# Performance work log

Hardware: AMD Instinct MI355X
Metric: run time of the kernel (lower is better)

## Reference

```python
import jax, jax.numpy as jnp
import numpy as np

B, T, D = 2, 128, 1024
H, R, Dk, Dv = 8, 8, 64, 64


def setup_inputs() -> dict:
    key = jax.random.key(0)
    ks = jax.random.split(key, 11)
    w = lambda k, shp: jax.random.normal(k, shp, dtype=jnp.float32) * 0.02
    return {
        "hidden_states": jax.random.normal(ks[0], (B, T, D), dtype=jnp.float32),
        "Wq": w(ks[1], (D, H * Dk)),
        "Wk": w(ks[2], (D, H * Dk)),
        "Wv": w(ks[3], (D, H * Dv)),
        "Wb": w(ks[4], (D, H * R)),
        "Wtg": w(ks[5], (D, H * R)),
        "mode_logits": jax.random.normal(ks[6], (H, R), dtype=jnp.float32) * 0.1,
        "log_decay": jax.random.normal(ks[7], (H, R), dtype=jnp.float32) * 0.1,
        "omega_log_scale": jax.random.normal(ks[8], (H, R), dtype=jnp.float32) * 0.1,
        "Wg": w(ks[9], (D, H * Dv)),
        "Wo": w(ks[10], (H * Dv, D)),
    }


def _forward(x, Wq, Wk, Wv, Wb, Wtg, mode_logits, log_decay, omega_log_scale, Wg, Wo):
    b, t, _ = x.shape
    # projections
    q = (x @ Wq).reshape(b, t, H, Dk)
    k = (x @ Wk).reshape(b, t, H, Dk)
    v = (x @ Wv).reshape(b, t, H, Dv)
    beta = jax.nn.sigmoid((x @ Wb).reshape(b, t, H, R))
    tg = jax.nn.sigmoid((x @ Wtg).reshape(b, t, H, R))
    # spectral mode parameters
    pair_idx = jnp.arange(0, Dk, 2, dtype=jnp.float32)
    inv_freq = 1.0 / (10000.0 ** (pair_idx / Dk))            # [Dk/2]
    omega = jnp.exp(omega_log_scale)[..., None] * inv_freq    # [H,R,Dk/2]
    omega_full = jnp.repeat(omega, 2, axis=-1)                # [H,R,Dk] (repeat_interleave)
    cos_w = jnp.cos(omega_full)[None, :, :, None, :]          # [1,H,R,1,Dk]
    sin_w = jnp.sin(omega_full)[None, :, :, None, :]
    rho = jnp.exp(-jax.nn.softplus(log_decay))                # [H,R]
    mode_w = jax.nn.softmax(mode_logits, axis=-1)             # [H,R]

    # time-major for scan
    qT = jnp.moveaxis(q, 1, 0)
    kT = jnp.moveaxis(k, 1, 0)
    vT = jnp.moveaxis(v, 1, 0)
    betaT = jnp.moveaxis(beta, 1, 0)
    tgT = jnp.moveaxis(tg, 1, 0)

    def step(carry, xs):
        sr, si = carry                      # [B,H,R,Dv,Dk] each
        q_t, k_t, v_t, b_t, g_t = xs
        decay = (g_t * rho)[..., None, None]            # [B,H,R,1,1]
        rot_r = decay * (cos_w * sr - sin_w * si)
        rot_i = decay * (sin_w * sr + cos_w * si)
        pred = jnp.einsum('bhrvk,bhk->bhrv', rot_r, k_t)
        err = v_t[:, :, None, :] - pred                  # [B,H,R,Dv]
        write = err[..., None] * k_t[:, :, None, None, :]
        sr_new = rot_r + b_t[..., None, None] * write
        read = jnp.einsum('bhrvk,bhk->bhrv', sr_new, q_t)
        y = jnp.einsum('bhrv,hr->bhv', read, mode_w)     # [B,H,Dv]
        return (sr_new, rot_i), y

    s0 = jnp.zeros((b, H, R, Dv, Dk), dtype=x.dtype)
    _, ys = jax.lax.scan(step, (s0, s0), (qT, kT, vT, betaT, tgT))
    o = jnp.moveaxis(ys, 0, 1)                           # [B,T,H,Dv]
    gate = jax.nn.sigmoid((x @ Wg).reshape(b, t, H, Dv))
    o = (o * gate).reshape(b, t, H * Dv)
    return o @ Wo


def reference(hidden_states, Wq, Wk, Wv, Wb, Wtg, mode_logits, log_decay,
              omega_log_scale, Wg, Wo):
    return _forward(hidden_states, Wq, Wk, Wv, Wb, Wtg, mode_logits,
                    log_decay, omega_log_scale, Wg, Wo)
```

## Files before the change

kernel.cpp:

```cpp
#include <hip/hip_runtime.h>
#include <math.h>

#define T_ 128
#define NPROJ 2176
#define CH 32

typedef __attribute__((ext_vector_type(8))) short short8;
typedef __attribute__((ext_vector_type(4))) float float4v;
typedef __attribute__((ext_vector_type(2))) float float2v;

__device__ __forceinline__ ushort f2bf(float x) {
    unsigned u = __float_as_uint(x);
    u += 0x7FFF + ((u >> 16) & 1);
    return (ushort)(u >> 16);
}

template<int CTRL>
__device__ __forceinline__ float dpp_add(float x) {
    int xi = __float_as_int(x);
    int yi = __builtin_amdgcn_update_dpp(xi, xi, CTRL, 0xF, 0xF, false);
    return x + __int_as_float(yi);
}

__global__ __launch_bounds__(256) void prep_kernel(
    const float* __restrict__ x,
    const float* __restrict__ Wq, const float* __restrict__ Wk,
    const float* __restrict__ Wv, const float* __restrict__ Wb,
    const float* __restrict__ Wtg, const float* __restrict__ Wg,
    const float* __restrict__ Wo,
    const float* __restrict__ mode_logits, const float* __restrict__ log_decay,
    const float* __restrict__ ols,
    float* __restrict__ cosw, float* __restrict__ sinw,
    float* __restrict__ rho, float* __restrict__ modew,
    ushort* __restrict__ xb, ushort* __restrict__ wtb, ushort* __restrict__ wotb,
    float* __restrict__ Acomb)
{
    __shared__ ushort tile[64][68];
    const int blk = blockIdx.x, tid = threadIdx.x;
    if (blk < 16) {
        int idx = blk * 256 + tid;
        if (idx >= 64 * 64) return;
        int t = idx >> 6;
        int k = idx & 63;
        int h = t >> 3;
        if (k == 0) {
            float ld = log_decay[t];
            rho[t] = 1.0f / (1.0f + expf(ld));
            float m = -1e30f;
            for (int i = 0; i < 8; i++) m = fmaxf(m, mode_logits[h * 8 + i]);
            float sum = 0.0f;
            for (int i = 0; i < 8; i++) sum += expf(mode_logits[h * 8 + i] - m);
            modew[t] = expf(mode_logits[t] - m) / sum;
        }
        float osc = expf(ols[t]);
        int p = k >> 1;
        float invf = expf(-((float)(2 * p) / 64.0f) * logf(10000.0f));
        float w = osc * invf;
        cosw[idx] = cosf(w);
        sinw[idx] = sinf(w);
        return;
    }
    if (blk < 80) {
        int base = (blk - 16) * 4096 + tid * 16;
        float4 f0 = *(const float4*)&x[base];
        float4 f1 = *(const float4*)&x[base + 4];
        float4 f2 = *(const float4*)&x[base + 8];
        float4 f3 = *(const float4*)&x[base + 12];
        short8 o0, o1;
        o0[0]=f2bf(f0.x); o0[1]=f2bf(f0.y); o0[2]=f2bf(f0.z); o0[3]=f2bf(f0.w);
        o0[4]=f2bf(f1.x); o0[5]=f2bf(f1.y); o0[6]=f2bf(f1.z); o0[7]=f2bf(f1.w);
        o1[0]=f2bf(f2.x); o1[1]=f2bf(f2.y); o1[2]=f2bf(f2.z); o1[3]=f2bf(f2.w);
        o1[4]=f2bf(f3.x); o1[5]=f2bf(f3.y); o1[6]=f2bf(f3.z); o1[7]=f2bf(f3.w);
        *(short8*)&xb[base] = o0;
        *(short8*)&xb[base + 8] = o1;
        return;
    }
    if (blk >= 752) {
        int base = (blk - 752) * 4096 + tid * 16;
        float4 z = make_float4(0.f, 0.f, 0.f, 0.f);
        *(float4*)&Acomb[base] = z;
        *(float4*)&Acomb[base + 4] = z;
        *(float4*)&Acomb[base + 8] = z;
        *(float4*)&Acomb[base + 12] = z;
        return;
    }
    const float* src; int ld, c0, n0, k0, ldd; ushort* dst;
    if (blk < 624) {
        int b3 = blk - 80; int nt = b3 >> 4, kt = b3 & 15;
        n0 = nt * 64; k0 = kt * 64;
        if (n0 < 512)       { src = Wq;  c0 = n0;        ld = 512; }
        else if (n0 < 1024) { src = Wk;  c0 = n0 - 512;  ld = 512; }
        else if (n0 < 1536) { src = Wv;  c0 = n0 - 1024; ld = 512; }
        else if (n0 < 1600) { src = Wb;  c0 = n0 - 1536; ld = 64;  }
        else if (n0 < 1664) { src = Wtg; c0 = n0 - 1600; ld = 64;  }
        else                { src = Wg;  c0 = n0 - 1664; ld = 512; }
        dst = wtb; ldd = 1024;
    } else {
        int b4 = blk - 624; int nt = b4 >> 3, kt = b4 & 7;
        n0 = nt * 64; k0 = kt * 64;
        src = Wo; c0 = n0; ld = 1024; dst = wotb; ldd = 512;
    }
    #pragma unroll
    for (int rep = 0; rep < 4; rep++) {
        int k = rep * 16 + (tid >> 4);
        int nc = (tid & 15) * 4;
        float4 f = *(const float4*)&src[(size_t)(k0 + k) * ld + c0 + nc];
        tile[nc + 0][k] = f2bf(f.x);
        tile[nc + 1][k] = f2bf(f.y);
        tile[nc + 2][k] = f2bf(f.z);
        tile[nc + 3][k] = f2bf(f.w);
    }
    __syncthreads();
    #pragma unroll
    for (int rep = 0; rep < 4; rep++) {
        int n = rep * 16 + (tid >> 4);
        int kc = (tid & 15) * 4;
        uint2 uu = *(const uint2*)&tile[n][kc];
        *(uint2*)&dst[(size_t)(n0 + n) * ldd + k0 + kc] = uu;
    }
}

__global__ __launch_bounds__(256, 2) void proj_mfma(const ushort* __restrict__ Ab,
        const ushort* __restrict__ BTb, const float* __restrict__ rho,
        float* __restrict__ proj)
{
    __shared__ ushort sA[2][64][40];
    __shared__ ushort sB[2][64][40];
    const int n0 = blockIdx.x * 64, m0 = blockIdx.y * 64;
    const int tid = threadIdx.x;
    const int lane = tid & 63, w = tid >> 6;
    const int wm = w & 1, wn = w >> 1;
    const int l16 = lane & 15, quad = lane >> 4;
    const int srow = tid >> 2, skq = (tid & 3) * 8;
    const ushort* Ag = Ab + (size_t)(m0 + srow) * 1024 + skq;
    const ushort* Bg = BTb + (size_t)(n0 + srow) * 1024 + skq;
    short8 raA = *(const short8*)Ag;
    short8 rbA = *(const short8*)Bg;
    short8 raB = *(const short8*)(Ag + 32);
    short8 rbB = *(const short8*)(Bg + 32);
    float4v acc00 = {0,0,0,0}, acc01 = {0,0,0,0}, acc10 = {0,0,0,0}, acc11 = {0,0,0,0};
    for (int kt = 0; kt < 32; kt += 2) {
        *(short8*)&sA[0][srow][skq] = raA;
        *(short8*)&sB[0][srow][skq] = rbA;
        __syncthreads();
        if (kt + 2 < 32) {
            raA = *(const short8*)(Ag + (kt + 2) * 32);
            rbA = *(const short8*)(Bg + (kt + 2) * 32);
        }
        {
            short8 a0 = *(const short8*)&sA[0][wm * 32 + l16][quad * 8];
            short8 a1 = *(const short8*)&sA[0][wm * 32 + 16 + l16][quad * 8];
            short8 b0 = *(const short8*)&sB[0][wn * 32 + l16][quad * 8];
            short8 b1 = *(const short8*)&sB[0][wn * 32 + 16 + l16][quad * 8];
            acc00 = __builtin_amdgcn_mfma_f32_16x16x32_bf16(a0, b0, acc00, 0, 0, 0);
            acc01 = __builtin_amdgcn_mfma_f32_16x16x32_bf16(a0, b1, acc01, 0, 0, 0);
            acc10 = __builtin_amdgcn_mfma_f32_16x16x32_bf16(a1, b0, acc10, 0, 0, 0);
            acc11 = __builtin_amdgcn_mfma_f32_16x16x32_bf16(a1, b1, acc11, 0, 0, 0);
        }
        *(short8*)&sA[1][srow][skq] = raB;
        *(short8*)&sB[1][srow][skq] = rbB;
        __syncthreads();
        if (kt + 3 < 32) {
            raB = *(const short8*)(Ag + (kt + 3) * 32);
            rbB = *(const short8*)(Bg + (kt + 3) * 32);
        }
        {
            short8 a0 = *(const short8*)&sA[1][wm * 32 + l16][quad * 8];
            short8 a1 = *(const short8*)&sA[1][wm * 32 + 16 + l16][quad * 8];
            short8 b0 = *(const short8*)&sB[1][wn * 32 + l16][quad * 8];
            short8 b1 = *(const short8*)&sB[1][wn * 32 + 16 + l16][quad * 8];
            acc00 = __builtin_amdgcn_mfma_f32_16x16x32_bf16(a0, b0, acc00, 0, 0, 0);
            acc01 = __builtin_amdgcn_mfma_f32_16x16x32_bf16(a0, b1, acc01, 0, 0, 0);
            acc10 = __builtin_amdgcn_mfma_f32_16x16x32_bf16(a1, b0, acc10, 0, 0, 0);
            acc11 = __builtin_amdgcn_mfma_f32_16x16x32_bf16(a1, b1, acc11, 0, 0, 0);
        }
    }
    const bool sig = (n0 >= 1536);
    float m0c = 1.0f, m1c = 1.0f;
    if (n0 == 1600) {
        m0c = rho[wn * 32 + l16];
        m1c = rho[wn * 32 + l16 + 16];
    }
    const int colb = n0 + wn * 32 + l16;
    const int rowb = m0 + wm * 32 + quad * 4;
    #pragma unroll
    for (int r2 = 0; r2 < 4; r2++) {
        float v00 = acc00[r2], v01 = acc01[r2], v10 = acc10[r2], v11 = acc11[r2];
        if (sig) {
            v00 = m0c / (1.0f + expf(-v00));
            v01 = m1c / (1.0f + expf(-v01));
            v10 = m0c / (1.0f + expf(-v10));
            v11 = m1c / (1.0f + expf(-v11));
        }
        proj[(size_t)(rowb + r2) * NPROJ + colb] = v00;
        proj[(size_t)(rowb + r2) * NPROJ + colb + 16] = v01;
        proj[(size_t)(rowb + 16 + r2) * NPROJ + colb] = v10;
        proj[(size_t)(rowb + 16 + r2) * NPROJ + colb + 16] = v11;
    }
}

__global__ __launch_bounds__(256, 2) void scan_kernel(const float* __restrict__ proj,
        const float* __restrict__ cosw, const float* __restrict__ sinw,
        const float* __restrict__ modew, float* __restrict__ Acomb)
{
    __shared__ float4 qks[2][CH][16][3];
    __shared__ float2 vg[2][CH][16];
    __shared__ float sc4[2][CH][4];
    __shared__ float obuf[CH][16];

    const int bi = blockIdx.x;
    const int s  = bi & 3;
    const int hr = (bi >> 2) & 63;
    const int b  = bi >> 8;
    const int h = hr >> 3;
    const int r = hr & 7;
    const int tid = threadIdx.x;
    const int vl = tid >> 4;
    const int kl = tid & 15;

    float2v cw0, cw1, sw0, sw1;
    cw0.x = cosw[hr * 64 + kl * 4 + 0]; cw0.y = cosw[hr * 64 + kl * 4 + 1];
    cw1.x = cosw[hr * 64 + kl * 4 + 2]; cw1.y = cosw[hr * 64 + kl * 4 + 3];
    sw0.x = sinw[hr * 64 + kl * 4 + 0]; sw0.y = sinw[hr * 64 + kl * 4 + 1];
    sw1.x = sinw[hr * 64 + kl * 4 + 2]; sw1.y = sinw[hr * 64 + kl * 4 + 3];
    const float mw = modew[hr];
    float2v sr0 = {0,0}, sr1 = {0,0}, si0 = {0,0}, si1 = {0,0};

    const float* pb = proj + (size_t)b * T_ * NPROJ;
    const int qbase = h * 64;
    const int kbase = 512 + h * 64;
    const int vbase = 1024 + h * 64 + s * 16;
    const int gbase = 1664 + h * 64 + s * 16;
    const int boff  = 1536 + h * 8 + r;
    const int goff  = 1600 + h * 8 + r;

    {
        #pragma unroll
        for (int rep = 0; rep < 4; rep++) {
            int idx = rep * 256 + tid;
            int t = idx >> 5, sub = idx & 31;
            const float* row = pb + (size_t)t * NPROJ;
            float4 f = *(const float4*)(row + (sub < 16 ? qbase + sub * 4
                                                        : kbase + (sub - 16) * 4));
            qks[0][t][sub & 15][sub < 16 ? 1 : 0] = f;
        }
        #pragma unroll
        for (int rep = 0; rep < 2; rep++) {
            int idx = rep * 256 + tid;
            int t = idx >> 4, v2 = idx & 15;
            const float* row = pb + (size_t)t * NPROJ;
            vg[0][t][v2] = make_float2(row[vbase + v2], row[gbase + v2]);
        }
        if (tid < CH)            sc4[0][tid][0]      = pb[(size_t)tid * NPROJ + boff];
        else if (tid < 2 * CH)   sc4[0][tid - CH][1] = pb[(size_t)(tid - CH) * NPROJ + goff];
    }
    __syncthreads();

    float* dstb = Acomb + ((size_t)b * 128) * 512 + h * 64 + s * 16;

    for (int c = 0; c < T_ / CH; c++) {
        const int cb = c & 1, nb = cb ^ 1;
        const bool have = (c + 1 < T_ / CH);

        float4 g_qk[4]; float2 g_vg[2]; float g_sc = 0.0f;
        if (have) {
            const int t0 = (c + 1) * CH;
            #pragma unroll
            for (int rep = 0; rep < 4; rep++) {
                int idx = rep * 256 + tid;
                int t = idx >> 5, sub = idx & 31;
                const float* row = pb + (size_t)(t0 + t) * NPROJ;
                g_qk[rep] = *(const float4*)(row + (sub < 16 ? qbase + sub * 4
                                                             : kbase + (sub - 16) * 4));
            }
            #pragma unroll
            for (int rep = 0; rep < 2; rep++) {
                int idx = rep * 256 + tid;
                int t = idx >> 4, v2 = idx & 15;
                const float* row = pb + (size_t)(t0 + t) * NPROJ;
                g_vg[rep] = make_float2(row[vbase + v2], row[gbase + v2]);
            }
            if (tid < CH)          g_sc = pb[(size_t)(t0 + tid) * NPROJ + boff];
            else if (tid < 2 * CH) g_sc = pb[(size_t)(t0 + tid - CH) * NPROJ + goff];
        }

        {
            int t = tid >> 3, j = tid & 7;
            float4 ka = qks[cb][t][2 * j][0];
            float4 qa = qks[cb][t][2 * j][1];
            float4 kb = qks[cb][t][2 * j + 1][0];
            float4 qb = qks[cb][t][2 * j + 1][1];
            float p = ka.x * qa.x + ka.y * qa.y + ka.z * qa.z + ka.w * qa.w
                    + kb.x * qb.x + kb.y * qb.y + kb.z * qb.z + kb.w * qb.w;
            p = dpp_add<0xB1>(p);
            p = dpp_add<0x4E>(p);
            p = dpp_add<0x141>(p);
            if (j == 0) sc4[cb][t][2] = p;
        }
        if (c > 0) {
            #pragma unroll
            for (int rep = 0; rep < 2; rep++) {
                int idx = rep * 256 + tid;
                int t = idx >> 4, v2 = idx & 15;
                atomicAdd(dstb + (size_t)((c - 1) * CH + t) * 512 + v2, obuf[t][v2]);
            }
        }
        __syncthreads();

        const float2* vgb = &vg[cb][0][0];
        const float4* svb = (const float4*)&sc4[cb][0][0];

        float4 kvp[2], qvp[2], svp[2]; float2 vgp[2];
        kvp[0] = qks[cb][0][kl][0]; qvp[0] = qks[cb][0][kl][1];
        svp[0] = svb[0];            vgp[0] = vgb[vl];
        kvp[1] = qks[cb][1][kl][0]; qvp[1] = qks[cb][1][kl][1];
        svp[1] = svb[1];            vgp[1] = vgb[16 + vl];

        #pragma unroll
        for (int t = 0; t < CH; t++) {
            const int cur = t & 1;
            float4 kv = kvp[cur], qv = qvp[cur], sv = svp[cur];
            float2 vgv = vgp[cur];
            if (t + 2 < CH) {
                kvp[cur] = qks[cb][t + 2][kl][0];
                qvp[cur] = qks[cb][t + 2][kl][1];
                svp[cur] = svb[t + 2];
                vgp[cur] = vgb[(t + 2) * 16 + vl];
            }

            float2v k0; k0.x = kv.x; k0.y = kv.y;
            float2v k1; k1.x = kv.z; k1.y = kv.w;
            float2v q0; q0.x = qv.x; q0.y = qv.y;
            float2v q1; q1.x = qv.z; q1.y = qv.w;

            const float decay = sv.y;
            float2v t1 = cw0 * sr0 - sw0 * si0;
            float2v u1 = sw0 * sr0 + cw0 * si0;
            float2v t2 = cw1 * sr1 - sw1 * si1;
            float2v u2 = sw1 * sr1 + cw1 * si1;
            float2v d2; d2.x = decay; d2.y = decay;
            float2v rr0 = d2 * t1, rr1 = d2 * t2;
            si0 = d2 * u1; si1 = d2 * u2;

            float2v pk2 = rr0 * k0 + rr1 * k1;
            float2v pq2 = rr0 * q0 + rr1 * q1;
            float pk = pk2.x + pk2.y;
            float pq = pq2.x + pq2.y;
            pk = dpp_add<0xB1>(pk);  pq = dpp_add<0xB1>(pq);
            pk = dpp_add<0x4E>(pk);  pq = dpp_add<0x4E>(pq);
            pk = dpp_add<0x141>(pk); pq = dpp_add<0x141>(pq);
            pk = dpp_add<0x140>(pk); pq = dpp_add<0x140>(pq);

            const float sc = sv.x * (vgv.x - pk);
            float2v sc2; sc2.x = sc; sc2.y = sc;
            sr0 = rr0 + sc2 * k0;
            sr1 = rr1 + sc2 * k1;
            const float rp = pq + sc * sv.z;
            if (kl == 0) obuf[t][vl] = mw * rp * vgv.y;
        }

        if (have) {
            #pragma unroll
            for (int rep = 0; rep < 4; rep++) {
                int idx = rep * 256 + tid;
                int t = idx >> 5, sub = idx & 31;
                qks[nb][t][sub & 15][sub < 16 ? 1 : 0] = g_qk[rep];
            }
            #pragma unroll
            for (int rep = 0; rep < 2; rep++) {
                int idx = rep * 256 + tid;
                int t = idx >> 4, v2 = idx & 15;
                vg[nb][t][v2] = g_vg[rep];
            }
            if (tid < CH)          sc4[nb][tid][0]      = g_sc;
            else if (tid < 2 * CH) sc4[nb][tid - CH][1] = g_sc;
        }
        __syncthreads();
    }
    #pragma unroll
    for (int rep = 0; rep < 2; rep++) {
        int idx = rep * 256 + tid;
        int t = idx >> 4, v2 = idx & 15;
        atomicAdd(dstb + (size_t)(3 * CH + t) * 512 + v2, obuf[t][v2]);
    }
}

__global__ __launch_bounds__(256, 2) void out_mfma(const float* __restrict__ Af,
        const ushort* __restrict__ BTb, float* __restrict__ C)
{
    __shared__ ushort sA[2][64][40];
    __shared__ ushort sB[2][64][40];
    const int n0 = blockIdx.x * 64, m0 = blockIdx.y * 64;
    const int tid = threadIdx.x;
    const int lane = tid & 63, w = tid >> 6;
    const int wm = w & 1, wn = w >> 1;
    const int l16 = lane & 15, quad = lane >> 4;
    const int srow = tid >> 2, skq = (tid & 3) * 8;
    const float* Ag = Af + (size_t)(m0 + srow) * 512 + skq;
    const ushort* Bg = BTb + (size_t)(n0 + srow) * 512 + skq;
    float4 fa0A = *(const float4*)Ag;
    float4 fa1A = *(const float4*)(Ag + 4);
    short8 rbA  = *(const short8*)Bg;
    float4 fa0B = *(const float4*)(Ag + 32);
    float4 fa1B = *(const float4*)(Ag + 36);
    short8 rbB  = *(const short8*)(Bg + 32);
    float4v acc00 = {0,0,0,0}, acc01 = {0,0,0,0}, acc10 = {0,0,0,0}, acc11 = {0,0,0,0};
    for (int kt = 0; kt < 16; kt += 2) {
        {
            short8 ra;
            ra[0]=f2bf(fa0A.x); ra[1]=f2bf(fa0A.y); ra[2]=f2bf(fa0A.z); ra[3]=f2bf(fa0A.w);
            ra[4]=f2bf(fa1A.x); ra[5]=f2bf(fa1A.y); ra[6]=f2bf(fa1A.z); ra[7]=f2bf(fa1A.w);
            *(short8*)&sA[0][srow][skq] = ra;
            *(short8*)&sB[0][srow][skq] = rbA;
        }
        __syncthreads();
        if (kt + 2 < 16) {
            fa0A = *(const float4*)(Ag + (kt + 2) * 32);
            fa1A = *(const float4*)(Ag + (kt + 2) * 32 + 4);
            rbA  = *(const short8*)(Bg + (kt + 2) * 32);
        }
        {
            short8 a0 = *(const short8*)&sA[0][wm * 32 + l16][quad * 8];
            short8 a1 = *(const short8*)&sA[0][wm * 32 + 16 + l16][quad * 8];
            short8 b0 = *(const short8*)&sB[0][wn * 32 + l16][quad * 8];
            short8 b1 = *(const short8*)&sB[0][wn * 32 + 16 + l16][quad * 8];
            acc00 = __builtin_amdgcn_mfma_f32_16x16x32_bf16(a0, b0, acc00, 0, 0, 0);
            acc01 = __builtin_amdgcn_mfma_f32_16x16x32_bf16(a0, b1, acc01, 0, 0, 0);
            acc10 = __builtin_amdgcn_mfma_f32_16x16x32_bf16(a1, b0, acc10, 0, 0, 0);
            acc11 = __builtin_amdgcn_mfma_f32_16x16x32_bf16(a1, b1, acc11, 0, 0, 0);
        }
        {
            short8 ra;
            ra[0]=f2bf(fa0B.x); ra[1]=f2bf(fa0B.y); ra[2]=f2bf(fa0B.z); ra[3]=f2bf(fa0B.w);
            ra[4]=f2bf(fa1B.x); ra[5]=f2bf(fa1B.y); ra[6]=f2bf(fa1B.z); ra[7]=f2bf(fa1B.w);
            *(short8*)&sA[1][srow][skq] = ra;
            *(short8*)&sB[1][srow][skq] = rbB;
        }
        __syncthreads();
        if (kt + 3 < 16) {
            fa0B = *(const float4*)(Ag + (kt + 3) * 32);
            fa1B = *(const float4*)(Ag + (kt + 3) * 32 + 4);
            rbB  = *(const short8*)(Bg + (kt + 3) * 32);
        }
        {
            short8 a0 = *(const short8*)&sA[1][wm * 32 + l16][quad * 8];
            short8 a1 = *(const short8*)&sA[1][wm * 32 + 16 + l16][quad * 8];
            short8 b0 = *(const short8*)&sB[1][wn * 32 + l16][quad * 8];
            short8 b1 = *(const short8*)&sB[1][wn * 32 + 16 + l16][quad * 8];
            acc00 = __builtin_amdgcn_mfma_f32_16x16x32_bf16(a0, b0, acc00, 0, 0, 0);
            acc01 = __builtin_amdgcn_mfma_f32_16x16x32_bf16(a0, b1, acc01, 0, 0, 0);
            acc10 = __builtin_amdgcn_mfma_f32_16x16x32_bf16(a1, b0, acc10, 0, 0, 0);
            acc11 = __builtin_amdgcn_mfma_f32_16x16x32_bf16(a1, b1, acc11, 0, 0, 0);
        }
    }
    const int colb = n0 + wn * 32 + l16;
    const int rowb = m0 + wm * 32 + quad * 4;
    #pragma unroll
    for (int r2 = 0; r2 < 4; r2++) {
        C[(size_t)(rowb + r2) * 1024 + colb] = acc00[r2];
        C[(size_t)(rowb + r2) * 1024 + colb + 16] = acc01[r2];
        C[(size_t)(rowb + 16 + r2) * 1024 + colb] = acc10[r2];
        C[(size_t)(rowb + 16 + r2) * 1024 + colb + 16] = acc11[r2];
    }
}

extern "C" void kernel_launch(void* const* d_in, const int* in_sizes, int n_in,
                              void* d_out, int out_size, void* d_ws, size_t ws_size,
                              hipStream_t stream) {
    const float* x   = (const float*)d_in[0];
    const float* Wq  = (const float*)d_in[1];
    const float* Wk  = (const float*)d_in[2];
    const float* Wv  = (const float*)d_in[3];
    const float* Wb  = (const float*)d_in[4];
    const float* Wtg = (const float*)d_in[5];
    const float* ml  = (const float*)d_in[6];
    const float* ldc = (const float*)d_in[7];
    const float* ols = (const float*)d_in[8];
    const float* Wg  = (const float*)d_in[9];
    const float* Wo  = (const float*)d_in[10];
    float* out = (float*)d_out;

    float* ws = (float*)d_ws;
    float* proj    = ws;
    float* cosw    = proj + 256 * NPROJ;
    float* sinw    = cosw + 4096;
    float* rho     = sinw + 4096;
    float* modew   = rho + 64;
    ushort* xb     = (ushort*)(modew + 64);
    ushort* wotb   = (ushort*)((float*)xb + 131072);
    float*  Acomb  = (float*)wotb + 262144;
    ushort* wtb    = (ushort*)(Acomb + 131072);

    prep_kernel<<<784, 256, 0, stream>>>(x, Wq, Wk, Wv, Wb, Wtg, Wg, Wo,
                                         ml, ldc, ols, cosw, sinw, rho, modew,
                                         xb, wtb, wotb, Acomb);
    proj_mfma<<<dim3(34, 4), 256, 0, stream>>>(xb, wtb, rho, proj);
    scan_kernel<<<512, 256, 0, stream>>>(proj, cosw, sinw, modew, Acomb);
    out_mfma<<<dim3(16, 4), 256, 0, stream>>>(Acomb, wotb, out);
}
```

Before: 155.8 us.

## Replace sequential scan with chunked WY-style delta-rule using MFMA

Replaces the per-timestep recurrent state update in the scan kernel with a chunked formulation. Each chunk of 32 steps builds rotated k/q fragments, forms intra-chunk Gram matrices with bf16 MFMA, solves a triangular system for the correction terms, and carries inter-chunk state in split hi/lo bf16 fragments. This aims to turn the serial per-step dependency chain into matrix multiplies and halves the grid. In exchange it adds bf16 rounding error, cos/sin evaluation per element, a serial triangular solve on one wave, and cumulative-log decay scaling that could overflow or underflow.

```diff
diff --git a/kernel.cpp b/kernel.cpp
--- a/kernel.cpp
+++ b/kernel.cpp
@@ -7,20 +7,14 @@
 
 typedef __attribute__((ext_vector_type(8))) short short8;
 typedef __attribute__((ext_vector_type(4))) float float4v;
-typedef __attribute__((ext_vector_type(2))) float float2v;
+typedef __attribute__((ext_vector_type(16))) float f32x16;
 
 __device__ __forceinline__ ushort f2bf(float x) {
     unsigned u = __float_as_uint(x);
     u += 0x7FFF + ((u >> 16) & 1);
     return (ushort)(u >> 16);
 }
-
-template<int CTRL>
-__device__ __forceinline__ float dpp_add(float x) {
-    int xi = __float_as_int(x);
-    int yi = __builtin_amdgcn_update_dpp(xi, xi, CTRL, 0xF, 0xF, false);
-    return x + __int_as_float(yi);
-}
+__device__ __forceinline__ float bfu(ushort u) { return __uint_as_float(((unsigned)u) << 16); }
 
 __global__ __launch_bounds__(256) void prep_kernel(
     const float* __restrict__ x,
@@ -30,7 +24,7 @@
     const float* __restrict__ Wo,
     const float* __restrict__ mode_logits, const float* __restrict__ log_decay,
     const float* __restrict__ ols,
-    float* __restrict__ cosw, float* __restrict__ sinw,
+    float* __restrict__ cosw, float* __restrict__ sinw, float* __restrict__ omg,
     float* __restrict__ rho, float* __restrict__ modew,
     ushort* __restrict__ xb, ushort* __restrict__ wtb, ushort* __restrict__ wotb,
     float* __restrict__ Acomb)
@@ -58,6 +52,7 @@
         float w = osc * invf;
         cosw[idx] = cosf(w);
         sinw[idx] = sinf(w);
+        omg[idx] = w;
         return;
     }
     if (blk < 80) {
@@ -201,187 +196,250 @@
 
 __global__ __launch_bounds__(256, 2) void scan_kernel(const float* __restrict__ proj,
         const float* __restrict__ cosw, const float* __restrict__ sinw,
-        const float* __restrict__ modew, float* __restrict__ Acomb)
+        const float* __restrict__ omg, const float* __restrict__ modew,
+        float* __restrict__ Acomb)
 {
-    __shared__ float4 qks[2][CH][16][3];
-    __shared__ float2 vg[2][CH][16];
-    __shared__ float sc4[2][CH][4];
-    __shared__ float obuf[CH][16];
+    __shared__ float omgl[64], cw64[64], sw64[64], c31x[64], s31x[64];
+    __shared__ float bvec[32], ldl[32], lcp[32];
+    __shared__ float vpl[32][33];
+    __shared__ float Mm[32][36];
+    __shared__ float T1k[32][33];
+    __shared__ short8 fragKc[4][64], fragKs[4][64], fragQc[4][64], fragQs[4][64];
+    __shared__ short8 fragZ[4][4][64];
+    __shared__ short8 fragW[2][2][2][64];
+    __shared__ short8 fragA[2][64];
+    __shared__ short8 fragN[2][64];
 
     const int bi = blockIdx.x;
-    const int s  = bi & 3;
-    const int hr = (bi >> 2) & 63;
-    const int b  = bi >> 8;
-    const int h = hr >> 3;
-    const int r = hr & 7;
+    const int vh = bi & 1;
+    const int hr = (bi >> 1) & 63;
+    const int b  = bi >> 7;
+    const int h = hr >> 3, r = hr & 7;
     const int tid = threadIdx.x;
-    const int vl = tid >> 4;
-    const int kl = tid & 15;
-
-    float2v cw0, cw1, sw0, sw1;
-    cw0.x = cosw[hr * 64 + kl * 4 + 0]; cw0.y = cosw[hr * 64 + kl * 4 + 1];
-    cw1.x = cosw[hr * 64 + kl * 4 + 2]; cw1.y = cosw[hr * 64 + kl * 4 + 3];
-    sw0.x = sinw[hr * 64 + kl * 4 + 0]; sw0.y = sinw[hr * 64 + kl * 4 + 1];
-    sw1.x = sinw[hr * 64 + kl * 4 + 2]; sw1.y = sinw[hr * 64 + kl * 4 + 3];
+    const int wid = tid >> 6, lane = tid & 63;
+    const int l31 = lane & 31, hi = lane >> 5;
+
+    const float* pb = proj + (size_t)b * T_ * NPROJ;
+    const int qcol = h * 64;
+    const int kcol = 512 + h * 64;
+    const int vcol = 1024 + h * 64 + vh * 32;
+    const int gcol = 1664 + h * 64 + vh * 32;
+    const int bcol = 1536 + h * 8 + r;
+    const int dcol = 1600 + h * 8 + r;
     const float mw = modew[hr];
-    float2v sr0 = {0,0}, sr1 = {0,0}, si0 = {0,0}, si1 = {0,0};
-
-    const float* pb = proj + (size_t)b * T_ * NPROJ;
-    const int qbase = h * 64;
-    const int kbase = 512 + h * 64;
-    const int vbase = 1024 + h * 64 + s * 16;
-    const int gbase = 1664 + h * 64 + s * 16;
-    const int boff  = 1536 + h * 8 + r;
-    const int goff  = 1600 + h * 8 + r;
-
-    {
+
+    if (tid < 64) {
+        int k = tid;
+        float w = omg[hr * 64 + k];
+        omgl[k] = w;
+        cw64[k] = cosw[hr * 64 + k];
+        sw64[k] = sinw[hr * 64 + k];
+        c31x[k] = cosf(31.0f * w);
+        s31x[k] = sinf(31.0f * w);
+    }
+    for (int i = tid; i < 4 * 4 * 64 * 4; i += 256) ((float*)fragZ)[i] = 0.0f;
+    __syncthreads();
+
+    for (int c = 0; c < 4; c++) {
+        const int t0 = c * 32;
+        f32x16 accT;
         #pragma unroll
-        for (int rep = 0; rep < 4; rep++) {
-            int idx = rep * 256 + tid;
-            int t = idx >> 5, sub = idx & 31;
-            const float* row = pb + (size_t)t * NPROJ;
-            float4 f = *(const float4*)(row + (sub < 16 ? qbase + sub * 4
-                                                        : kbase + (sub - 16) * 4));
-            qks[0][t][sub & 15][sub < 16 ? 1 : 0] = f;
-        }
-        #pragma unroll
-        for (int rep = 0; rep < 2; rep++) {
-            int idx = rep * 256 + tid;
-            int t = idx >> 4, v2 = idx & 15;
-            const float* row = pb + (size_t)t * NPROJ;
-            vg[0][t][v2] = make_float2(row[vbase + v2], row[gbase + v2]);
-        }
-        if (tid < CH)            sc4[0][tid][0]      = pb[(size_t)tid * NPROJ + boff];
-        else if (tid < 2 * CH)   sc4[0][tid - CH][1] = pb[(size_t)(tid - CH) * NPROJ + goff];
-    }
-    __syncthreads();
-
-    float* dstb = Acomb + ((size_t)b * 128) * 512 + h * 64 + s * 16;
-
-    for (int c = 0; c < T_ / CH; c++) {
-        const int cb = c & 1, nb = cb ^ 1;
-        const bool have = (c + 1 < T_ / CH);
-
-        float4 g_qk[4]; float2 g_vg[2]; float g_sc = 0.0f;
-        if (have) {
-            const int t0 = (c + 1) * CH;
-            #pragma unroll
-            for (int rep = 0; rep < 4; rep++) {
-                int idx = rep * 256 + tid;
-                int t = idx >> 5, sub = idx & 31;
-                const float* row = pb + (size_t)(t0 + t) * NPROJ;
-                g_qk[rep] = *(const float4*)(row + (sub < 16 ? qbase + sub * 4
-                                                             : kbase + (sub - 16) * 4));
-            }
-            #pragma unroll
-            for (int rep = 0; rep < 2; rep++) {
-                int idx = rep * 256 + tid;
-                int t = idx >> 4, v2 = idx & 15;
-                const float* row = pb + (size_t)(t0 + t) * NPROJ;
-                g_vg[rep] = make_float2(row[vbase + v2], row[gbase + v2]);
-            }
-            if (tid < CH)          g_sc = pb[(size_t)(t0 + tid) * NPROJ + boff];
-            else if (tid < 2 * CH) g_sc = pb[(size_t)(t0 + tid - CH) * NPROJ + goff];
-        }
-
-        {
-            int t = tid >> 3, j = tid & 7;
-            float4 ka = qks[cb][t][2 * j][0];
-            float4 qa = qks[cb][t][2 * j][1];
-            float4 kb = qks[cb][t][2 * j + 1][0];
-            float4 qb = qks[cb][t][2 * j + 1][1];
-            float p = ka.x * qa.x + ka.y * qa.y + ka.z * qa.z + ka.w * qa.w
-                    + kb.x * qb.x + kb.y * qb.y + kb.z * qb.z + kb.w * qb.w;
-            p = dpp_add<0xB1>(p);
-            p = dpp_add<0x4E>(p);
-            p = dpp_add<0x141>(p);
-            if (j == 0) sc4[cb][t][2] = p;
-        }
-        if (c > 0) {
-            #pragma unroll
-            for (int rep = 0; rep < 2; rep++) {
-                int idx = rep * 256 + tid;
-                int t = idx >> 4, v2 = idx & 15;
-                atomicAdd(dstb + (size_t)((c - 1) * CH + t) * 512 + v2, obuf[t][v2]);
-            }
-        }
-        __syncthreads();
-
-        const float2* vgb = &vg[cb][0][0];
-        const float4* svb = (const float4*)&sc4[cb][0][0];
-
-        float4 kvp[2], qvp[2], svp[2]; float2 vgp[2];
-        kvp[0] = qks[cb][0][kl][0]; qvp[0] = qks[cb][0][kl][1];
-        svp[0] = svb[0];            vgp[0] = vgb[vl];
-        kvp[1] = qks[cb][1][kl][0]; qvp[1] = qks[cb][1][kl][1];
-        svp[1] = svb[1];            vgp[1] = vgb[16 + vl];
-
-        #pragma unroll
-        for (int t = 0; t < CH; t++) {
-            const int cur = t & 1;
-            float4 kv = kvp[cur], qv = qvp[cur], sv = svp[cur];
-            float2 vgv = vgp[cur];
-            if (t + 2 < CH) {
-                kvp[cur] = qks[cb][t + 2][kl][0];
-                qvp[cur] = qks[cb][t + 2][kl][1];
-                svp[cur] = svb[t + 2];
-                vgp[cur] = vgb[(t + 2) * 16 + vl];
-            }
-
-            float2v k0; k0.x = kv.x; k0.y = kv.y;
-            float2v k1; k1.x = kv.z; k1.y = kv.w;
-            float2v q0; q0.x = qv.x; q0.y = qv.y;
-            float2v q1; q1.x = qv.z; q1.y = qv.w;
-
-            const float decay = sv.y;
-            float2v t1 = cw0 * sr0 - sw0 * si0;
-            float2v u1 = sw0 * sr0 + cw0 * si0;
-            float2v t2 = cw1 * sr1 - sw1 * si1;
-            float2v u2 = sw1 * sr1 + cw1 * si1;
-            float2v d2; d2.x = decay; d2.y = decay;
-            float2v rr0 = d2 * t1, rr1 = d2 * t2;
-            si0 = d2 * u1; si1 = d2 * u2;
-
-            float2v pk2 = rr0 * k0 + rr1 * k1;
-            float2v pq2 = rr0 * q0 + rr1 * q1;
-            float pk = pk2.x + pk2.y;
-            float pq = pq2.x + pq2.y;
-            pk = dpp_add<0xB1>(pk);  pq = dpp_add<0xB1>(pq);
-            pk = dpp_add<0x4E>(pk);  pq = dpp_add<0x4E>(pq);
-            pk = dpp_add<0x141>(pk); pq = dpp_add<0x141>(pq);
-            pk = dpp_add<0x140>(pk); pq = dpp_add<0x140>(pq);
-
-            const float sc = sv.x * (vgv.x - pk);
-            float2v sc2; sc2.x = sc; sc2.y = sc;
-            sr0 = rr0 + sc2 * k0;
-            sr1 = rr1 + sc2 * k1;
-            const float rp = pq + sc * sv.z;
-            if (kl == 0) obuf[t][vl] = mw * rp * vgv.y;
-        }
-
-        if (have) {
-            #pragma unroll
-            for (int rep = 0; rep < 4; rep++) {
-                int idx = rep * 256 + tid;
-                int t = idx >> 5, sub = idx & 31;
-                qks[nb][t][sub & 15][sub < 16 ? 1 : 0] = g_qk[rep];
-            }
-            #pragma unroll
-            for (int rep = 0; rep < 2; rep++) {
-                int idx = rep * 256 + tid;
-                int t = idx >> 4, v2 = idx & 15;
-                vg[nb][t][v2] = g_vg[rep];
-            }
-            if (tid < CH)          sc4[nb][tid][0]      = g_sc;
-            else if (tid < 2 * CH) sc4[nb][tid - CH][1] = g_sc;
-        }
-        __syncthreads();
-    }
-    #pragma unroll
-    for (int rep = 0; rep < 2; rep++) {
-        int idx = rep * 256 + tid;
-        int t = idx >> 4, v2 = idx & 15;
-        atomicAdd(dstb + (size_t)(3 * CH + t) * 512 + v2, obuf[t][v2]);
+        for (int i = 0; i < 16; i++) accT[i] = 0.0f;
+
+        if (tid < 32) {
+            int t = tid;
+            bvec[t] = pb[(size_t)(t0 + t) * NPROJ + bcol];
+            ldl[t]  = log2f(pb[(size_t)(t0 + t) * NPROJ + dcol]);
+        }
+        {
+            int t = tid >> 3, vq = (tid & 7) * 4;
+            float4 f = *(const float4*)(pb + (size_t)(t0 + t) * NPROJ + vcol + vq);
+            vpl[t][vq + 0] = f.x; vpl[t][vq + 1] = f.y;
+            vpl[t][vq + 2] = f.z; vpl[t][vq + 3] = f.w;
+        }
+        __syncthreads();
+
+        if (tid == 0) {
+            float acc = ldl[0]; lcp[0] = acc;
+            for (int t = 1; t < 32; t++) { acc += ldl[t]; lcp[t] = acc; }
+        }
+        {
+            const int t = tid >> 3, k0 = (tid & 7) * 8;
+            const float ft = (float)t;
+            const float* rk = pb + (size_t)(t0 + t) * NPROJ + kcol + k0;
+            const float* rq = pb + (size_t)(t0 + t) * NPROJ + qcol + k0;
+            short8 kc8, ks8, qc8, qs8;
+            #pragma unroll
+            for (int j = 0; j < 8; j++) {
+                float w = omgl[k0 + j];
+                float ang = w * ft;
+                float cth = cosf(ang), sth = sinf(ang);
+                float kv = rk[j], qv = rq[j];
+                kc8[j] = (short)f2bf(cth * kv); ks8[j] = (short)f2bf(sth * kv);
+                qc8[j] = (short)f2bf(cth * qv); qs8[j] = (short)f2bf(sth * qv);
+            }
+            const int sI = k0 >> 4, ld_ = t + 32 * ((k0 >> 3) & 1);
+            fragKc[sI][ld_] = kc8; fragKs[sI][ld_] = ks8;
+            fragQc[sI][ld_] = qc8; fragQs[sI][ld_] = qs8;
+        }
+        __syncthreads();
+
+        if (wid == 3) {
+            f32x16 acc;
+            #pragma unroll
+            for (int i = 0; i < 16; i++) acc[i] = 0.0f;
+            #pragma unroll
+            for (int s = 0; s < 4; s++) {
+                short8 a = fragKc[s][lane];
+                acc = __builtin_amdgcn_mfma_f32_32x32x16_bf16(a, a, acc, 0, 0, 0);
+                short8 bq = fragKs[s][lane];
+                acc = __builtin_amdgcn_mfma_f32_32x32x16_bf16(bq, bq, acc, 0, 0, 0);
+            }
+            #pragma unroll
+            for (int reg = 0; reg < 16; reg++) {
+                int t = (reg & 3) + 8 * (reg >> 2) + 4 * hi;
+                float val = 0.0f;
+                if (l31 < t) val = bvec[t] * acc[reg] * exp2f(lcp[t] - lcp[l31]);
+                Mm[t][l31] = val;
+            }
+        } else if (wid == 1) {
+            f32x16 acc;
+            #pragma unroll
+            for (int i = 0; i < 16; i++) acc[i] = 0.0f;
+            #pragma unroll
+            for (int s = 0; s < 4; s++) {
+                acc = __builtin_amdgcn_mfma_f32_32x32x16_bf16(fragQc[s][lane], fragKc[s][lane], acc, 0, 0, 0);
+                acc = __builtin_amdgcn_mfma_f32_32x32x16_bf16(fragQs[s][lane], fragKs[s][lane], acc, 0, 0, 0);
+            }
+            #pragma unroll
+            for (int reg = 0; reg < 16; reg++) {
+                int t = (reg & 3) + 8 * (reg >> 2) + 4 * hi;
+                int ta = l31;
+                float val = (ta <= t) ? acc[reg] * exp2f(lcp[t] - lcp[ta]) : 0.0f;
+                ((ushort*)&fragN[ta >> 4][t + 32 * ((ta >> 3) & 1)])[ta & 7] = f2bf(val);
+            }
+            #pragma unroll
+            for (int s = 0; s < 4; s++) {
+                accT = __builtin_amdgcn_mfma_f32_32x32x16_bf16(fragQc[s][lane], fragZ[0][s][lane], accT, 0, 0, 0);
+                accT = __builtin_amdgcn_mfma_f32_32x32x16_bf16(fragQc[s][lane], fragZ[1][s][lane], accT, 0, 0, 0);
+                accT = __builtin_amdgcn_mfma_f32_32x32x16_bf16(fragQs[s][lane], fragZ[2][s][lane], accT, 0, 0, 0);
+                accT = __builtin_amdgcn_mfma_f32_32x32x16_bf16(fragQs[s][lane], fragZ[3][s][lane], accT, 0, 0, 0);
+            }
+        } else if (wid == 2) {
+            f32x16 acc;
+            #pragma unroll
+            for (int i = 0; i < 16; i++) acc[i] = 0.0f;
+            #pragma unroll
+            for (int s = 0; s < 4; s++) {
+                acc = __builtin_amdgcn_mfma_f32_32x32x16_bf16(fragKc[s][lane], fragZ[0][s][lane], acc, 0, 0, 0);
+                acc = __builtin_amdgcn_mfma_f32_32x32x16_bf16(fragKc[s][lane], fragZ[1][s][lane], acc, 0, 0, 0);
+                acc = __builtin_amdgcn_mfma_f32_32x32x16_bf16(fragKs[s][lane], fragZ[2][s][lane], acc, 0, 0, 0);
+                acc = __builtin_amdgcn_mfma_f32_32x32x16_bf16(fragKs[s][lane], fragZ[3][s][lane], acc, 0, 0, 0);
+            }
+            #pragma unroll
+            for (int reg = 0; reg < 16; reg++) {
+                int t = (reg & 3) + 8 * (reg >> 2) + 4 * hi;
+                T1k[t][l31] = acc[reg] * exp2f(lcp[t]);
+            }
+        } else {
+            for (int u = lane; u < 256; u += 64) {
+                int k = u & 63, so = u >> 6;
+                float w = omgl[k];
+                float lcpE = lcp[31];
+                short8 wr8, wi8;
+                #pragma unroll
+                for (int j = 0; j < 8; j++) {
+                    int ta = so * 8 + j;
+                    float pw = exp2f(lcpE - lcp[ta]);
+                    float kv = pb[(size_t)(t0 + ta) * NPROJ + kcol + k];
+                    float ang = w * (float)(31 - ta);
+                    wr8[j] = (short)f2bf(pw * cosf(ang) * kv);
+                    wi8[j] = (short)f2bf(pw * sinf(ang) * kv);
+                }
+                int tile = k >> 5, sm = so >> 1, ld_ = (k & 31) + 32 * (so & 1);
+                fragW[0][tile][sm][ld_] = wr8;
+                fragW[1][tile][sm][ld_] = wi8;
+            }
+        }
+        __syncthreads();
+
+        if (wid == 3) {
+            float areg[32];
+            #pragma unroll
+            for (int i = 0; i < 32; i++) areg[i] = 0.0f;
+            const int v = l31;
+            #pragma unroll
+            for (int t = 0; t < 32; t++) {
+                float p = 0.0f;
+                #pragma unroll
+                for (int t4 = 0; t4 < t; t4 += 4) {
+                    float4 m4 = *(const float4*)&Mm[t][t4];
+                    p += m4.x * areg[t4] + m4.y * areg[t4 + 1]
+                       + m4.z * areg[t4 + 2] + m4.w * areg[t4 + 3];
+                }
+                float at = bvec[t] * (vpl[t][v] - T1k[t][v]) - p;
+                areg[t] = at;
+                if (hi == ((t >> 3) & 1))
+                    ((ushort*)&fragA[t >> 4][l31 + 32 * ((t >> 3) & 1)])[t & 7] = f2bf(at);
+            }
+        }
+        __syncthreads();
+
+        if (wid == 1) {
+            #pragma unroll
+            for (int reg = 0; reg < 16; reg++) {
+                int t = (reg & 3) + 8 * (reg >> 2) + 4 * hi;
+                accT[reg] *= exp2f(lcp[t]);
+            }
+            accT = __builtin_amdgcn_mfma_f32_32x32x16_bf16(fragN[0][lane], fragA[0][lane], accT, 0, 0, 0);
+            accT = __builtin_amdgcn_mfma_f32_32x32x16_bf16(fragN[1][lane], fragA[1][lane], accT, 0, 0, 0);
+            #pragma unroll
+            for (int reg = 0; reg < 16; reg++) {
+                int t = (reg & 3) + 8 * (reg >> 2) + 4 * hi;
+                int v = l31;
+                float g = pb[(size_t)(t0 + t) * NPROJ + gcol + v];
+                atomicAdd(Acomb + ((size_t)(b * 128 + t0 + t)) * 512 + h * 64 + vh * 32 + v,
+                          mw * accT[reg] * g);
+            }
+        } else if (wid == 0 || wid == 2) {
+            const int tile = (wid == 0) ? 0 : 1;
+            const int k = tile * 32 + l31;
+            const int sIz = k >> 4, jz = k & 7, hbk = (k >> 3) & 1;
+            const float cpE = exp2f(lcp[31]);
+            const float c31v = c31x[k], s31v = s31x[k];
+            const float cwv = cw64[k], swv = sw64[k];
+            f32x16 aR, aI;
+            #pragma unroll
+            for (int reg = 0; reg < 16; reg++) {
+                int v = (reg & 3) + 8 * (reg >> 2) + 4 * hi;
+                int lf = v + 32 * hbk;
+                float yr = bfu(((ushort*)&fragZ[0][sIz][lf])[jz]) + bfu(((ushort*)&fragZ[1][sIz][lf])[jz]);
+                float yn = bfu(((ushort*)&fragZ[2][sIz][lf])[jz]) + bfu(((ushort*)&fragZ[3][sIz][lf])[jz]);
+                float yi = -yn;
+                aR[reg] = cpE * (c31v * yr - s31v * yi);
+                aI[reg] = cpE * (s31v * yr + c31v * yi);
+            }
+            aR = __builtin_amdgcn_mfma_f32_32x32x16_bf16(fragA[0][lane], fragW[0][tile][0][lane], aR, 0, 0, 0);
+            aR = __builtin_amdgcn_mfma_f32_32x32x16_bf16(fragA[1][lane], fragW[0][tile][1][lane], aR, 0, 0, 0);
+            aI = __builtin_amdgcn_mfma_f32_32x32x16_bf16(fragA[0][lane], fragW[1][tile][0][lane], aI, 0, 0, 0);
+            aI = __builtin_amdgcn_mfma_f32_32x32x16_bf16(fragA[1][lane], fragW[1][tile][1][lane], aI, 0, 0, 0);
+            #pragma unroll
+            for (int reg = 0; reg < 16; reg++) {
+                int v = (reg & 3) + 8 * (reg >> 2) + 4 * hi;
+                int lf = v + 32 * hbk;
+                float zr = aR[reg], zi = aI[reg];
+                float yrn = cwv * zr - swv * zi;
+                float yin = swv * zr + cwv * zi;
+                float nyi = -yin;
+                ushort rh = f2bf(yrn);
+                ushort ih = f2bf(nyi);
+                ((ushort*)&fragZ[0][sIz][lf])[jz] = rh;
+                ((ushort*)&fragZ[1][sIz][lf])[jz] = f2bf(yrn - bfu(rh));
+                ((ushort*)&fragZ[2][sIz][lf])[jz] = ih;
+                ((ushort*)&fragZ[3][sIz][lf])[jz] = f2bf(nyi - bfu(ih));
+            }
+        }
+        __syncthreads();
     }
 }
 
@@ -490,11 +548,12 @@
     ushort* wotb   = (ushort*)((float*)xb + 131072);
     float*  Acomb  = (float*)wotb + 262144;
     ushort* wtb    = (ushort*)(Acomb + 131072);
+    float*  omg    = (float*)(wtb + 2228224);
 
     prep_kernel<<<784, 256, 0, stream>>>(x, Wq, Wk, Wv, Wb, Wtg, Wg, Wo,
-                                         ml, ldc, ols, cosw, sinw, rho, modew,
+                                         ml, ldc, ols, cosw, sinw, omg, rho, modew,
                                          xb, wtb, wotb, Acomb);
     proj_mfma<<<dim3(34, 4), 256, 0, stream>>>(xb, wtb, rho, proj);
-    scan_kernel<<<512, 256, 0, stream>>>(proj, cosw, sinw, modew, Acomb);
+    scan_kernel<<<256, 256, 0, stream>>>(proj, cosw, sinw, omg, modew, Acomb);
     out_mfma<<<dim3(16, 4), 256, 0, stream>>>(Acomb, wotb, out);
 }
```

New measurement: 179.4 us. 1.15x slower.
